# Kernel optimization log

Measured on AMD Instinct MI355X. Metric: run time of the kernel, lower is better.

Reference implementation:

```python
import jax, jax.numpy as jnp
from jax import lax
import numpy as np

C = 256       # residual_channels == skip_channels
B = 4
T = 4096
LATENT = 128
NB = 4        # n_blocks
NL = 10       # n_layers
ENC_DILS = tuple(2 ** i for i in range(NL)) * NB   # 40 encoder blocks
DEC_DILS = tuple(2 ** i for i in range(NL))        # 10 decoder blocks


def causal_conv(x, W, b, d):
    # x: [B, Cin, T], W: [Cout, Cin, k], left-pad by (k-1)*d for causality
    pad = (W.shape[-1] - 1) * d
    y = lax.conv_general_dilated(x, W, (1,), [(pad, 0)], rhs_dilation=(d,),
                                 dimension_numbers=('NCH', 'OIH', 'NCH'))
    return y + b[None, :, None]


def gated_block(h, Wf, bf, Wg, bg, Wr, br, Ws, bs, d):
    f = jnp.tanh(causal_conv(h, Wf, bf, d))
    g = jax.nn.sigmoid(causal_conv(h, Wg, bg, d))
    out = f * g
    res = jnp.einsum('oc,bct->bot', Wr, out) + br[None, :, None] + h
    skip = jnp.einsum('oc,bct->bot', Ws, out) + bs[None, :, None]
    return res, skip


def setup_inputs() -> dict:
    key = jax.random.key(0)
    ks = jax.random.split(key, 24)
    s = 0.05
    nE = NB * NL
    d = {}
    d['x'] = jax.random.normal(ks[0], (B, 1, T), jnp.float32)
    d['eps'] = jax.random.normal(ks[1], (B, LATENT), jnp.float32)
    d['enc_in_W'] = jax.random.normal(ks[2], (C, 1, 2)) * s
    d['enc_in_b'] = jnp.zeros((C,), jnp.float32)
    d['enc_Wf'] = jax.random.normal(ks[3], (nE, C, C, 2)) * s
    d['enc_bf'] = jnp.zeros((nE, C), jnp.float32)
    d['enc_Wg'] = jax.random.normal(ks[4], (nE, C, C, 2)) * s
    d['enc_bg'] = jnp.zeros((nE, C), jnp.float32)
    d['enc_Wr'] = jax.random.normal(ks[5], (nE, C, C)) * s
    d['enc_br'] = jnp.zeros((nE, C), jnp.float32)
    d['enc_Ws'] = jax.random.normal(ks[6], (nE, C, C)) * s
    d['enc_bs'] = jnp.zeros((nE, C), jnp.float32)
    d['fc_mu_W'] = jax.random.normal(ks[7], (LATENT, C)) * s
    d['fc_mu_b'] = jnp.zeros((LATENT,), jnp.float32)
    d['fc_lv_W'] = jax.random.normal(ks[8], (LATENT, C)) * s
    d['fc_lv_b'] = jnp.zeros((LATENT,), jnp.float32)
    d['dec_in_W'] = jax.random.normal(ks[9], (C, LATENT)) * s
    d['dec_in_b'] = jnp.zeros((C,), jnp.float32)
    d['dec_Wf'] = jax.random.normal(ks[10], (NL, C, C, 2)) * s
    d['dec_bf'] = jnp.zeros((NL, C), jnp.float32)
    d['dec_Wg'] = jax.random.normal(ks[11], (NL, C, C, 2)) * s
    d['dec_bg'] = jnp.zeros((NL, C), jnp.float32)
    d['dec_Wr'] = jax.random.normal(ks[12], (NL, C, C)) * s
    d['dec_br'] = jnp.zeros((NL, C), jnp.float32)
    d['out_W'] = jax.random.normal(ks[13], (1, C)) * s
    d['out_b'] = jnp.zeros((1,), jnp.float32)
    return d


def _forward(x, eps, enc_in_W, enc_in_b, enc_Wf, enc_bf, enc_Wg, enc_bg,
             enc_Wr, enc_br, enc_Ws, enc_bs, fc_mu_W, fc_mu_b, fc_lv_W, fc_lv_b,
             dec_in_W, dec_in_b, dec_Wf, dec_bf, dec_Wg, dec_bg, dec_Wr, dec_br,
             out_W, out_b):
    # --- encode ---
    h = causal_conv(x, enc_in_W, enc_in_b, 1)
    skip_sum = jnp.zeros((h.shape[0], C, h.shape[2]), h.dtype)
    for i, dil in enumerate(ENC_DILS):
        h, skip = gated_block(h, enc_Wf[i], enc_bf[i], enc_Wg[i], enc_bg[i],
                              enc_Wr[i], enc_br[i], enc_Ws[i], enc_bs[i], dil)
        skip_sum = skip_sum + skip
    pooled = skip_sum.mean(axis=-1)                      # [B, C]
    mu = pooled @ fc_mu_W.T + fc_mu_b                    # [B, LATENT]
    logvar = pooled @ fc_lv_W.T + fc_lv_b
    # --- reparameterize ---
    z = mu + eps * jnp.exp(0.5 * logvar)
    # --- decode (length-1 sequence) ---
    h2 = (jnp.einsum('ol,bl->bo', dec_in_W, z) + dec_in_b)[:, :, None]  # [B, C, 1]
    for i, dil in enumerate(DEC_DILS):
        f = jnp.tanh(causal_conv(h2, dec_Wf[i], dec_bf[i], dil))
        g = jax.nn.sigmoid(causal_conv(h2, dec_Wg[i], dec_bg[i], dil))
        out = f * g
        h2 = jnp.einsum('oc,bct->bot', dec_Wr[i], out) + dec_br[i][None, :, None] + h2
    y = jnp.einsum('oc,bct->bot', out_W, h2) + out_b[None, :, None]     # [B, 1, 1]
    return (y, mu, logvar)


def reference(x, eps, enc_in_W, enc_in_b, enc_Wf, enc_bf, enc_Wg, enc_bg,
              enc_Wr, enc_br, enc_Ws, enc_bs, fc_mu_W, fc_mu_b, fc_lv_W, fc_lv_b,
              dec_in_W, dec_in_b, dec_Wf, dec_bf, dec_Wg, dec_bg, dec_Wr, dec_br,
              out_W, out_b):
    return _forward(x, eps, enc_in_W, enc_in_b, enc_Wf, enc_bf, enc_Wg, enc_bg,
                    enc_Wr, enc_br, enc_Ws, enc_bs, fc_mu_W, fc_mu_b, fc_lv_W, fc_lv_b,
                    dec_in_W, dec_in_b, dec_Wf, dec_bf, dec_Wg, dec_bg, dec_Wr, dec_br,
                    out_W, out_b)
```

## Files before the change

### kernel.cpp

```cpp
#include <hip/hip_runtime.h>

typedef unsigned short u16;
typedef __attribute__((ext_vector_type(8))) __bf16 bf16x8;
typedef __attribute__((ext_vector_type(4))) float f32x4;

constexpr int C = 256;
constexpr int T = 4096;
constexpr int B = 4;
constexpr int NENC = 40;
constexpr int NDEC = 10;
constexpr int TILE = 64;

__device__ __forceinline__ float bf2f(u16 v) {
  union { unsigned u; float f; } x;
  x.u = ((unsigned)v) << 16;
  return x.f;
}
__device__ __forceinline__ u16 f2bf(float f) {
  union { float ff; unsigned u; } x;
  x.ff = f;
  unsigned r = x.u + 0x7fffu + ((x.u >> 16) & 1u);
  return (u16)(r >> 16);
}
__device__ __forceinline__ int swz(int row, int col) {
  int g = ((row & 7) ^ (row >> 3)) & 7;
  return row * 512 + (col ^ (g << 3));
}

typedef __attribute__((address_space(1))) const unsigned int* gp1_t;
typedef __attribute__((address_space(3))) unsigned int* lp3_t;
__device__ __forceinline__ void gl_lds16(const u16* g, u16* l) {
  __builtin_amdgcn_global_load_lds((gp1_t)(const void*)g, (lp3_t)(void*)l, 16, 0, 0);
}

__global__ void k_pack1(const float* __restrict__ Wf, const float* __restrict__ Wg,
                        u16* __restrict__ penc1, int total) {
  int p = blockIdx.x * 256 + threadIdx.x;
  if (p >= total) return;
  int lane = p & 63;
  int s = (p >> 6) & 3;
  int c = (p >> 8) & 15;
  int wv = (p >> 12) & 7;
  int layer = p >> 15;
  int co = wv * 32 + (s & 1) * 16 + (lane & 15);
  int k = c * 32 + (lane >> 4) * 8;
  const float* src = (s >= 2 ? Wg : Wf) + ((size_t)layer * C + co) * 512 + k;
  u16* dst = penc1 + (size_t)p * 8;
#pragma unroll
  for (int r = 0; r < 8; ++r) dst[r] = f2bf(src[r]);
}

__global__ void k_pack2(const float* __restrict__ Wr, u16* __restrict__ penc2, int total) {
  int p = blockIdx.x * 256 + threadIdx.x;
  if (p >= total) return;
  int lane = p & 63;
  int s = (p >> 6) & 1;
  int c = (p >> 7) & 7;
  int wv = (p >> 10) & 7;
  int layer = p >> 13;
  int co = wv * 32 + s * 16 + (lane & 15);
  int k = c * 32 + (lane >> 4) * 8;
  const float* src = Wr + ((size_t)layer * C + co) * 256 + k;
  u16* dst = penc2 + (size_t)p * 8;
#pragma unroll
  for (int r = 0; r < 8; ++r) dst[r] = f2bf(src[r]);
}

__global__ void k_packd(const float* __restrict__ dWf, const float* __restrict__ dWg,
                        const float* __restrict__ dWr, const float* __restrict__ dinW,
                        u16* __restrict__ pdfg, u16* __restrict__ pdr,
                        u16* __restrict__ tdin) {
  int p = blockIdx.x * 256 + threadIdx.x;
  if (p < 163840) {
    int lane = p & 63;
    int s = (p >> 6) & 1;
    int c = (p >> 7) & 7;
    int wv = (p >> 10) & 15;
    int layer = p >> 14;
    int co = wv * 16 + (lane & 15);
    int k = c * 32 + (lane >> 4) * 8;
    const float* src = (s ? dWg : dWf) + (((size_t)(layer * C + co)) * C + k) * 2 + 1;
    u16* dst = pdfg + (size_t)p * 8;
#pragma unroll
    for (int r = 0; r < 8; ++r) dst[r] = f2bf(src[2 * r]);
  } else if (p < 245760) {
    int q = p - 163840;
    int lane = q & 63;
    int c = (q >> 6) & 7;
    int wv = (q >> 9) & 15;
    int layer = q >> 13;
    int co = wv * 16 + (lane & 15);
    int k = c * 32 + (lane >> 4) * 8;
    const float* src = dWr + ((size_t)(layer * C + co)) * C + k;
    u16* dst = pdr + (size_t)q * 8;
#pragma unroll
    for (int r = 0; r < 8; ++r) dst[r] = f2bf(src[r]);
  } else if (p < 249856) {
    int u = p - 245760;
#pragma unroll
    for (int r = 0; r < 8; ++r) tdin[u * 8 + r] = f2bf(dinW[u * 8 + r]);
  }
}

__global__ void k_zero(float* __restrict__ p, int n) {
  int i = blockIdx.x * 256 + threadIdx.x;
  if (i < n) p[i] = 0.f;
}

__global__ void k_input(const float* __restrict__ x, const float* __restrict__ W,
                        const float* __restrict__ bin, float* __restrict__ h) {
  int idx = blockIdx.x * 256 + threadIdx.x;
  int t = idx & (T - 1);
  int c = (idx >> 12) & (C - 1);
  int b = idx >> 20;
  float xv = x[b * T + t];
  float xp = (t > 0) ? x[b * T + t - 1] : 0.f;
  h[idx] = W[2 * c] * xp + W[2 * c + 1] * xv + bin[c];
}

__global__ __launch_bounds__(512, 2) void k_enc(
    const float* __restrict__ hin, float* __restrict__ hout, float* __restrict__ rowsum_l,
    const u16* __restrict__ pw1, const float* __restrict__ bfb,
    const float* __restrict__ bgb,
    const u16* __restrict__ pw2, const float* __restrict__ brb,
    int dil) {
  extern __shared__ __align__(16) u16 smem[];
  u16* wb = smem + 64 * 512;
  const int tid = threadIdx.x;
  const int wave = tid >> 6;
  const int lane = tid & 63;
  const int ncol = lane & 15;
  const int quad = lane >> 4;
  const int wg = blockIdx.x;
  const int b = wg >> 6;
  const int t0 = (wg & 63) * TILE;
  const float* hb = hin + b * C * T;

  const int co0 = wave * 32;
  const int kq = quad * 8;
  const int off1 = (wg >> 3) & 15;
  const int off2 = (wg >> 3) & 7;
  const u16* b1 = pw1 + wave * 32768 + lane * 8;
  const u16* b2 = pw2 + wave * 8192 + lane * 8;
  u16* wreg0 = wb + wave * 2048;
  u16* wreg1 = wb + 16384 + wave * 2048;
  const int aoff = lane * 8;

#pragma unroll
  for (int cc = 0; cc < 2; ++cc) {
    u16* ld = cc ? wreg1 : wreg0;
    const u16* gs = b1 + ((off1 + cc) & 15) * 2048;
    gl_lds16(gs, ld);
    gl_lds16(gs + 512, ld + 512);
    gl_lds16(gs + 1024, ld + 1024);
    gl_lds16(gs + 1536, ld + 1536);
  }

  const int n4 = tid & 15;
  const int cib = tid >> 4;
  float4 v[16];
  const bool al4 = ((dil & 3) == 0);
  if (t0 >= dil) {
#pragma unroll
    for (int it2 = 0; it2 < 16; ++it2) {
      int ci = (cib + it2 * 32) & 255;
      int tap = it2 >> 3;
      int tb = t0 + n4 * 4 - (tap ? 0 : dil);
      const float* p = hb + ci * T + tb;
      if (tap || al4) {
        v[it2] = *(const float4*)p;
      } else {
        v[it2].x = p[0]; v[it2].y = p[1]; v[it2].z = p[2]; v[it2].w = p[3];
      }
    }
  } else {
#pragma unroll
    for (int it2 = 0; it2 < 16; ++it2) {
      int ci = (cib + it2 * 32) & 255;
      int tap = it2 >> 3;
      int tb = t0 + n4 * 4 - (tap ? 0 : dil);
      const float* p = hb + ci * T + tb;
      if (tap) {
        v[it2] = *(const float4*)p;
      } else {
        v[it2].x = (tb + 0 >= 0) ? p[0] : 0.f;
        v[it2].y = (tb + 1 >= 0) ? p[1] : 0.f;
        v[it2].z = (tb + 2 >= 0) ? p[2] : 0.f;
        v[it2].w = (tb + 3 >= 0) ? p[3] : 0.f;
      }
    }
  }
#pragma unroll
  for (int it2 = 0; it2 < 8; ++it2) {
    int ci = (cib + it2 * 32) & 255;
    const float* p0 = (const float*)&v[it2];
    const float* p1 = (const float*)&v[it2 + 8];
#pragma unroll
    for (int r = 0; r < 4; ++r) {
      unsigned w32 = (unsigned)f2bf(p0[r]) | ((unsigned)f2bf(p1[r]) << 16);
      *(unsigned*)(&smem[swz(n4 * 4 + r, 2 * ci)]) = w32;
    }
  }
  __syncthreads();

  f32x4 acc[4][4];
#pragma unroll
  for (int m = 0; m < 4; ++m)
#pragma unroll
    for (int nt = 0; nt < 4; ++nt)
      acc[m][nt] = (f32x4){0.f, 0.f, 0.f, 0.f};

#pragma unroll
  for (int c = 0; c < 16; ++c) {
    if (c < 15) asm volatile("s_waitcnt vmcnt(4)" ::: "memory");
    else        asm volatile("s_waitcnt vmcnt(0)" ::: "memory");
    const u16* wr_ = (c & 1) ? wreg1 : wreg0;
    bf16x8 af0 = *(const bf16x8*)(wr_ + aoff);
    bf16x8 af1 = *(const bf16x8*)(wr_ + 512 + aoff);
    bf16x8 af2 = *(const bf16x8*)(wr_ + 1024 + aoff);
    bf16x8 af3 = *(const bf16x8*)(wr_ + 1536 + aoff);
    const int kk = ((c + off1) & 15) * 32 + kq;
    bf16x8 bfr[4];
#pragma unroll
    for (int nt = 0; nt < 4; ++nt)
      bfr[nt] = *(const bf16x8*)(&smem[swz(nt * 16 + ncol, kk)]);
#pragma unroll
    for (int nt = 0; nt < 4; ++nt) {
      acc[0][nt] = __builtin_amdgcn_mfma_f32_16x16x32_bf16(af0, bfr[nt], acc[0][nt], 0, 0, 0);
      acc[1][nt] = __builtin_amdgcn_mfma_f32_16x16x32_bf16(af1, bfr[nt], acc[1][nt], 0, 0, 0);
      acc[2][nt] = __builtin_amdgcn_mfma_f32_16x16x32_bf16(af2, bfr[nt], acc[2][nt], 0, 0, 0);
      acc[3][nt] = __builtin_amdgcn_mfma_f32_16x16x32_bf16(af3, bfr[nt], acc[3][nt], 0, 0, 0);
    }
    if (c + 2 < 16) {
      asm volatile("s_waitcnt lgkmcnt(0)" ::: "memory");
      u16* ld = (c & 1) ? wreg1 : wreg0;
      const u16* gs = b1 + ((c + 2 + off1) & 15) * 2048;
      gl_lds16(gs, ld);
      gl_lds16(gs + 512, ld + 512);
      gl_lds16(gs + 1024, ld + 1024);
      gl_lds16(gs + 1536, ld + 1536);
    }
  }

#pragma unroll
  for (int cc = 0; cc < 2; ++cc) {
    u16* ld = cc ? wreg1 : wreg0;
    const u16* gs = b2 + ((off2 + cc) & 7) * 1024;
    gl_lds16(gs, ld);
    gl_lds16(gs + 512, ld + 512);
  }
  __syncthreads();

  float* rsb = rowsum_l + b * C;
#pragma unroll
  for (int j = 0; j < 2; ++j) {
    const int cob = co0 + j * 16 + quad * 4;
    float bfv[4], bgv[4], rs[4];
#pragma unroll
    for (int r = 0; r < 4; ++r) {
      bfv[r] = bfb[cob + r];
      bgv[r] = bgb[cob + r];
      rs[r] = 0.f;
    }
#pragma unroll
    for (int nt = 0; nt < 4; ++nt) {
      const int n = nt * 16 + ncol;
      u16 pk[4];
#pragma unroll
      for (int r = 0; r < 4; ++r) {
        float fv = acc[j][nt][r] + bfv[r];
        float gv = acc[2 + j][nt][r] + bgv[r];
        float th = 1.f - 2.f / (__expf(2.f * fv) + 1.f);
        float sg = 1.f / (1.f + __expf(-gv));
        float o = th * sg;
        rs[r] += o;
        pk[r] = f2bf(o);
      }
      uint2 w;
      w.x = (unsigned)pk[0] | ((unsigned)pk[1] << 16);
      w.y = (unsigned)pk[2] | ((unsigned)pk[3] << 16);
      *(uint2*)(&smem[swz(n, cob)]) = w;
    }
#pragma unroll
    for (int r = 0; r < 4; ++r) {
      float s = rs[r];
      s += __shfl_xor(s, 1);
      s += __shfl_xor(s, 2);
      s += __shfl_xor(s, 4);
      s += __shfl_xor(s, 8);
      if (ncol == 0) atomicAdd(&rsb[cob + r], s);
    }
  }
  __syncthreads();

  f32x4 acc2[2][4];
#pragma unroll
  for (int m = 0; m < 2; ++m)
#pragma unroll
    for (int nt = 0; nt < 4; ++nt)
      acc2[m][nt] = (f32x4){0.f, 0.f, 0.f, 0.f};

#pragma unroll
  for (int c = 0; c < 8; ++c) {
    if (c < 7) asm volatile("s_waitcnt vmcnt(2)" ::: "memory");
    else       asm volatile("s_waitcnt vmcnt(0)" ::: "memory");
    const u16* wr_ = (c & 1) ? wreg1 : wreg0;
    bf16x8 af0 = *(const bf16x8*)(wr_ + aoff);
    bf16x8 af1 = *(const bf16x8*)(wr_ + 512 + aoff);
    const int kk = ((c + off2) & 7) * 32 + kq;
    bf16x8 bfr[4];
#pragma unroll
    for (int nt = 0; nt < 4; ++nt)
      bfr[nt] = *(const bf16x8*)(&smem[swz(nt * 16 + ncol, kk)]);
#pragma unroll
    for (int nt = 0; nt < 4; ++nt) {
      acc2[0][nt] = __builtin_amdgcn_mfma_f32_16x16x32_bf16(af0, bfr[nt], acc2[0][nt], 0, 0, 0);
      acc2[1][nt] = __builtin_amdgcn_mfma_f32_16x16x32_bf16(af1, bfr[nt], acc2[1][nt], 0, 0, 0);
    }
    if (c + 2 < 8) {
      asm volatile("s_waitcnt lgkmcnt(0)" ::: "memory");
      u16* ld = (c & 1) ? wreg1 : wreg0;
      const u16* gs = b2 + ((c + 2 + off2) & 7) * 1024;
      gl_lds16(gs, ld);
      gl_lds16(gs + 512, ld + 512);
    }
  }
  __syncthreads();

  float* fb = (float*)smem;
#pragma unroll
  for (int m = 0; m < 2; ++m) {
    const int cob = co0 + m * 16 + quad * 4;
#pragma unroll
    for (int nt = 0; nt < 4; ++nt) {
      const int t = nt * 16 + ncol;
#pragma unroll
      for (int r = 0; r < 4; ++r)
        fb[(cob + r) * 66 + t] = acc2[m][nt][r] + brb[cob + r];
    }
  }
  __syncthreads();
  float* ho = hout + b * C * T;
#pragma unroll
  for (int it2 = 0; it2 < 8; ++it2) {
    const int ci = cib + it2 * 32;
    const float* fr = fb + ci * 66 + n4 * 4;
    float4 o;
    o.x = fr[0] + v[it2 + 8].x;
    o.y = fr[1] + v[it2 + 8].y;
    o.z = fr[2] + v[it2 + 8].z;
    o.w = fr[3] + v[it2 + 8].w;
    *(float4*)(ho + ci * T + t0 + n4 * 4) = o;
  }
}

__global__ __launch_bounds__(256) void k_skip(
    const float* __restrict__ encWs, const float* __restrict__ encbs,
    const float* __restrict__ rowsum, float* __restrict__ pooled) {
  __shared__ float rs[B][C];
  const int l = blockIdx.x;
  const int co = threadIdx.x;
  for (int i = co; i < B * C; i += 256) rs[i >> 8][i & 255] = rowsum[l * B * C + i];
  __syncthreads();
  const float* Wrow = encWs + (size_t)l * C * C + co * C;
  float bs = encbs[l * C + co] * (float)T;
  float d[B] = {0.f, 0.f, 0.f, 0.f};
  for (int ci = 0; ci < C; ci += 4) {
    float4 w = *(const float4*)(Wrow + ci);
#pragma unroll
    for (int b = 0; b < B; ++b)
      d[b] += w.x * rs[b][ci] + w.y * rs[b][ci + 1] + w.z * rs[b][ci + 2] + w.w * rs[b][ci + 3];
  }
#pragma unroll
  for (int b = 0; b < B; ++b) atomicAdd(&pooled[b * C + co], d[b] + bs);
}

__global__ __launch_bounds__(256) void k_fc(
    const float* __restrict__ pooled,
    const float* __restrict__ muW, const float* __restrict__ mub,
    const float* __restrict__ lvW, const float* __restrict__ lvb,
    float* __restrict__ mlbuf, float* __restrict__ dout) {
  __shared__ float pm[B * C];
  const int tid = threadIdx.x;
  for (int i = tid; i < B * C; i += 256) pm[i] = pooled[i] * (1.f / (float)T);
  __syncthreads();
  const int waveG = blockIdx.x * 4 + (tid >> 6);
  const int lane = tid & 63;
  for (int j = 0; j < 16; ++j) {
    int d = waveG * 16 + j;
    int b = d >> 8, r = d & 255, which = r >> 7, l = r & 127;
    const float* Wrow = (which ? lvW : muW) + l * C;
    const float* p = pm + b * C;
    float s = Wrow[lane] * p[lane] + Wrow[lane + 64] * p[lane + 64] +
              Wrow[lane + 128] * p[lane + 128] + Wrow[lane + 192] * p[lane + 192];
#pragma unroll
    for (int off = 32; off; off >>= 1) s += __shfl_xor(s, off);
    if (lane == 0) {
      float val = s + (which ? lvb[l] : mub[l]);
      mlbuf[which * 512 + b * 128 + l] = val;
      dout[4 + which * 512 + b * 128 + l] = val;
    }
  }
}

__global__ __launch_bounds__(1024, 1) void k_dec(
    const float* __restrict__ mlbuf, const float* __restrict__ eps,
    const u16* __restrict__ tdin, const float* __restrict__ dinb,
    const u16* __restrict__ pdfg, const float* __restrict__ dbf,
    const float* __restrict__ dbg,
    const u16* __restrict__ pdr, const float* __restrict__ dbr,
    const float* __restrict__ outW, const float* __restrict__ outb,
    float* __restrict__ dout) {
  extern __shared__ __align__(16) u16 dsm[];
  __shared__ __align__(16) u16 Ah[16][264];
  __shared__ __align__(16) u16 Ao[16][264];
  __shared__ float h2f[4][256];
  __shared__ float outred[4];
  const int tid = threadIdx.x;
  const int wave = tid >> 6;
  const int lane = tid & 63;
  const int ncol = lane & 15;
  const int quad = lane >> 4;
  const int kq = quad * 8;
  const int co = wave * 16 + ncol;
  u16* wreg = dsm + wave * 4096;

  bf16x8 tdw[4];
  {
    const u16* wp = tdin + co * 128;
#pragma unroll
    for (int it = 0; it < 4; ++it) tdw[it] = *(const bf16x8*)(wp + it * 32 + kq);
  }

  if (tid < 512) {
    int b = tid >> 7, l = tid & 127;
    float mu = mlbuf[b * 128 + l];
    float lv = mlbuf[512 + b * 128 + l];
    Ah[b][l] = f2bf(mu + eps[b * 128 + l] * expf(0.5f * lv));
  }
  if (tid < 4) outred[tid] = 0.f;
  __syncthreads();

  {
    f32x4 acch = (f32x4){0.f, 0.f, 0.f, 0.f};
#pragma unroll
    for (int it = 0; it < 4; ++it) {
      bf16x8 af = *(const bf16x8*)(&Ah[ncol][it * 32 + kq]);
      acch = __builtin_amdgcn_mfma_f32_16x16x32_bf16(af, tdw[it], acch, 0, 0, 0);
    }
    __syncthreads();
    if (quad == 0) {
      float bias = dinb[co];
#pragma unroll
      for (int r = 0; r < 4; ++r) {
        float hv = acch[r] + bias;
        h2f[r][co] = hv;
        Ah[r][co] = f2bf(hv);
      }
    }
  }
  {
    const u16* fb = pdfg + wave * 8192 + lane * 8;
#pragma unroll
    for (int cc = 0; cc < 4; ++cc) {
      gl_lds16(fb + cc * 1024, wreg + cc * 1024);
      gl_lds16(fb + cc * 1024 + 512, wreg + cc * 1024 + 512);
    }
  }
  __syncthreads();

  for (int i = 0; i < NDEC; ++i) {
    const u16* fb = pdfg + (i * 16 + wave) * 8192 + lane * 8;
    const u16* rb = pdr + (i * 16 + wave) * 4096 + lane * 8;

    f32x4 accf = (f32x4){0.f, 0.f, 0.f, 0.f};
    f32x4 accg = (f32x4){0.f, 0.f, 0.f, 0.f};
#pragma unroll
    for (int c = 0; c < 8; ++c) {
      if (c == 4) asm volatile("s_waitcnt vmcnt(6)" ::: "memory");
      else if (c == 5) asm volatile("s_waitcnt vmcnt(4)" ::: "memory");
      else if (c == 6) asm volatile("s_waitcnt vmcnt(2)" ::: "memory");
      else if (c == 7) asm volatile("s_waitcnt vmcnt(0)" ::: "memory");
      const u16* bufp = wreg + (c & 3) * 1024;
      bf16x8 bf_ = *(const bf16x8*)(bufp + lane * 8);
      bf16x8 bg_ = *(const bf16x8*)(bufp + 512 + lane * 8);
      bf16x8 af = *(const bf16x8*)(&Ah[ncol][c * 32 + kq]);
      accf = __builtin_amdgcn_mfma_f32_16x16x32_bf16(af, bf_, accf, 0, 0, 0);
      accg = __builtin_amdgcn_mfma_f32_16x16x32_bf16(af, bg_, accg, 0, 0, 0);
      if (c < 4) {
        asm volatile("s_waitcnt lgkmcnt(0)" ::: "memory");
        gl_lds16(fb + (c + 4) * 1024, wreg + (c & 3) * 1024);
        gl_lds16(fb + (c + 4) * 1024 + 512, wreg + (c & 3) * 1024 + 512);
      }
    }
    asm volatile("s_waitcnt lgkmcnt(0)" ::: "memory");
#pragma unroll
    for (int cc = 0; cc < 4; ++cc) gl_lds16(rb + cc * 512, wreg + cc * 1024);

    if (quad == 0) {
      float bfv = dbf[i * C + co];
      float bgv = dbg[i * C + co];
#pragma unroll
      for (int r = 0; r < 4; ++r) {
        float fv = accf[r] + bfv;
        float gv = accg[r] + bgv;
        float th = 1.f - 2.f / (__expf(2.f * fv) + 1.f);
        float sg = 1.f / (1.f + __expf(-gv));
        Ao[r][co] = f2bf(th * sg);
      }
    }
    __syncthreads();

    f32x4 accr = (f32x4){0.f, 0.f, 0.f, 0.f};
#pragma unroll
    for (int c = 0; c < 8; ++c) {
      if (c == 4) asm volatile("s_waitcnt vmcnt(3)" ::: "memory");
      else if (c == 5) asm volatile("s_waitcnt vmcnt(2)" ::: "memory");
      else if (c == 6) asm volatile("s_waitcnt vmcnt(1)" ::: "memory");
      else if (c == 7) asm volatile("s_waitcnt vmcnt(0)" ::: "memory");
      bf16x8 br_ = *(const bf16x8*)(wreg + (c & 3) * 1024 + lane * 8);
      bf16x8 af = *(const bf16x8*)(&Ao[ncol][c * 32 + kq]);
      accr = __builtin_amdgcn_mfma_f32_16x16x32_bf16(af, br_, accr, 0, 0, 0);
      if (c < 4) {
        asm volatile("s_waitcnt lgkmcnt(0)" ::: "memory");
        gl_lds16(rb + (c + 4) * 512, wreg + (c & 3) * 1024);
      }
    }
    if (i + 1 < NDEC) {
      const u16* nfb = pdfg + ((i + 1) * 16 + wave) * 8192 + lane * 8;
      asm volatile("s_waitcnt lgkmcnt(0)" ::: "memory");
#pragma unroll
      for (int cc = 0; cc < 4; ++cc) {
        gl_lds16(nfb + cc * 1024, wreg + cc * 1024);
        gl_lds16(nfb + cc * 1024 + 512, wreg + cc * 1024 + 512);
      }
    }
    if (quad == 0) {
      float brv = dbr[i * C + co];
#pragma unroll
      for (int r = 0; r < 4; ++r) {
        float hv = h2f[r][co] + accr[r] + brv;
        h2f[r][co] = hv;
        Ah[r][co] = f2bf(hv);
      }
    }
    __syncthreads();
  }

  {
    int b = tid >> 8, c = tid & 255;
    float val = outW[c] * h2f[b][c];
#pragma unroll
    for (int off = 32; off; off >>= 1) val += __shfl_xor(val, off);
    if (lane == 0) atomicAdd(&outred[b], val);
  }
  __syncthreads();
  if (tid < 4) dout[tid] = outred[tid] + outb[0];
}

extern "C" void kernel_launch(void* const* d_in, const int* in_sizes, int n_in,
                              void* d_out, int out_size, void* d_ws, size_t ws_size,
                              hipStream_t stream) {
  const float* x      = (const float*)d_in[0];
  const float* eps    = (const float*)d_in[1];
  const float* encinW = (const float*)d_in[2];
  const float* encinb = (const float*)d_in[3];
  const float* encWf  = (const float*)d_in[4];
  const float* encbf  = (const float*)d_in[5];
  const float* encWg  = (const float*)d_in[6];
  const float* encbg  = (const float*)d_in[7];
  const float* encWr  = (const float*)d_in[8];
  const float* encbr  = (const float*)d_in[9];
  const float* encWs  = (const float*)d_in[10];
  const float* encbs  = (const float*)d_in[11];
  const float* muW    = (const float*)d_in[12];
  const float* mub    = (const float*)d_in[13];
  const float* lvW    = (const float*)d_in[14];
  const float* lvb    = (const float*)d_in[15];
  const float* dinW   = (const float*)d_in[16];
  const float* dinb   = (const float*)d_in[17];
  const float* dWf    = (const float*)d_in[18];
  const float* dbf    = (const float*)d_in[19];
  const float* dWg    = (const float*)d_in[20];
  const float* dbg    = (const float*)d_in[21];
  const float* dWr    = (const float*)d_in[22];
  const float* dbr    = (const float*)d_in[23];
  const float* outW   = (const float*)d_in[24];
  const float* outb   = (const float*)d_in[25];
  float* dout = (float*)d_out;

  char* ws = (char*)d_ws;
  float* hA = (float*)ws;
  float* hB = hA + (size_t)B * C * T;
  float* pooled = hB + (size_t)B * C * T;
  float* mlbuf = pooled + B * C;
  float* rowsum = mlbuf + 1024;
  u16* penc1 = (u16*)(rowsum + NENC * B * C);
  u16* penc2 = penc1 + (size_t)10485760;
  u16* pdfg = penc2 + (size_t)2621440;
  u16* pdr = pdfg + (size_t)1310720;
  u16* tdin = pdr + (size_t)655360;

  (void)hipFuncSetAttribute(reinterpret_cast<const void*>(k_enc),
                            hipFuncAttributeMaxDynamicSharedMemorySize, 131072);
  (void)hipFuncSetAttribute(reinterpret_cast<const void*>(k_dec),
                            hipFuncAttributeMaxDynamicSharedMemorySize, 131072);

  k_pack1<<<(1310720 + 255) / 256, 256, 0, stream>>>(encWf, encWg, penc1, 1310720);
  k_pack2<<<(327680 + 255) / 256, 256, 0, stream>>>(encWr, penc2, 327680);
  k_packd<<<(249856 + 255) / 256, 256, 0, stream>>>(dWf, dWg, dWr, dinW, pdfg, pdr, tdin);

  const int nZ = B * C + 1024 + NENC * B * C;
  k_zero<<<(nZ + 255) / 256, 256, 0, stream>>>(pooled, nZ);
  k_input<<<(B * C * T) / 256, 256, 0, stream>>>(x, encinW, encinb, hA);

  for (int i = 0; i < NENC; ++i) {
    const int dil = 1 << (i % 10);
    const float* hi = (i & 1) ? hB : hA;
    float* ho = (i & 1) ? hA : hB;
    k_enc<<<256, 512, 131072, stream>>>(
        hi, ho, rowsum + (size_t)i * B * C,
        penc1 + (size_t)i * 262144, encbf + (size_t)i * C,
        encbg + (size_t)i * C,
        penc2 + (size_t)i * 65536, encbr + (size_t)i * C,
        dil);
  }

  k_skip<<<NENC, 256, 0, stream>>>(encWs, encbs, rowsum, pooled);
  k_fc<<<16, 256, 0, stream>>>(pooled, muW, mub, lvW, lvb, mlbuf, dout);
  k_dec<<<1, 1024, 131072, stream>>>(mlbuf, eps, tdin, dinb, pdfg, dbf, dbg,
                                     pdr, dbr, outW, outb, dout);
}
```

Measured before the change: 1.287 ms.

## Spread decoder across 16 blocks with global barriers and packed bf16 converts

Replaces the single-block MFMA decoder with a 16-block kernel where each block owns 16 output channels, computes scalar dot products from register-held bf16 weights, and exchanges gate outputs and hidden state through global memory with an atomic grid barrier per half-layer. Decoder weights are repacked into a new transposed layout to match this access pattern. The encoder's bf16 conversions are replaced with the hardware packed convert instruction. This aims to cut the serial decoder latency by using more CUs, at the cost of 20 global barriers and a reliance on all 16 blocks being co-resident.

```diff
diff --git a/kernel.cpp b/kernel.cpp
--- a/kernel.cpp
+++ b/kernel.cpp
@@ -72,29 +72,36 @@
                         u16* __restrict__ tdin) {
   int p = blockIdx.x * 256 + threadIdx.x;
   if (p < 163840) {
-    int lane = p & 63;
-    int s = (p >> 6) & 1;
-    int c = (p >> 7) & 7;
-    int wv = (p >> 10) & 15;
-    int layer = p >> 14;
-    int co = wv * 16 + (lane & 15);
-    int k = c * 32 + (lane >> 4) * 8;
-    const float* src = (s ? dWg : dWf) + (((size_t)(layer * C + co)) * C + k) * 2 + 1;
-    u16* dst = pdfg + (size_t)p * 8;
-#pragma unroll
-    for (int r = 0; r < 8; ++r) dst[r] = f2bf(src[2 * r]);
+    int e0 = p * 8;
+    int layer = e0 >> 17;
+    int rem = e0 & 131071;
+    int co = rem >> 9;
+    int q = rem & 511;
+    int which = q >> 8;
+    int pos0 = q & 255;
+    const float* src = (which ? dWg : dWf) + ((size_t)(layer * 256 + co)) * 512 + 1;
+    u16* dst = pdfg + e0;
+#pragma unroll
+    for (int r = 0; r < 8; ++r) {
+      int pos = pos0 + r;
+      int k = ((pos & 15) << 4) | (pos >> 4);
+      dst[r] = f2bf(src[2 * k]);
+    }
   } else if (p < 245760) {
     int q = p - 163840;
-    int lane = q & 63;
-    int c = (q >> 6) & 7;
-    int wv = (q >> 9) & 15;
-    int layer = q >> 13;
-    int co = wv * 16 + (lane & 15);
-    int k = c * 32 + (lane >> 4) * 8;
-    const float* src = dWr + ((size_t)(layer * C + co)) * C + k;
-    u16* dst = pdr + (size_t)q * 8;
-#pragma unroll
-    for (int r = 0; r < 8; ++r) dst[r] = f2bf(src[r]);
+    int e0 = q * 8;
+    int layer = e0 >> 16;
+    int rem = e0 & 65535;
+    int co = rem >> 8;
+    int pos0 = rem & 255;
+    const float* src = dWr + ((size_t)(layer * 256 + co)) * 256;
+    u16* dst = pdr + e0;
+#pragma unroll
+    for (int r = 0; r < 8; ++r) {
+      int pos = pos0 + r;
+      int k = ((pos & 15) << 4) | (pos >> 4);
+      dst[r] = f2bf(src[k]);
+    }
   } else if (p < 249856) {
     int u = p - 245760;
 #pragma unroll
@@ -197,7 +204,8 @@
     const float* p1 = (const float*)&v[it2 + 8];
 #pragma unroll
     for (int r = 0; r < 4; ++r) {
-      unsigned w32 = (unsigned)f2bf(p0[r]) | ((unsigned)f2bf(p1[r]) << 16);
+      unsigned w32;
+      asm("v_cvt_pk_bf16_f32 %0, %1, %2" : "=v"(w32) : "v"(p0[r]), "v"(p1[r]));
       *(unsigned*)(&smem[swz(n4 * 4 + r, 2 * ci)]) = w32;
     }
   }
@@ -255,7 +263,7 @@
 #pragma unroll
   for (int j = 0; j < 2; ++j) {
     const int cob = co0 + j * 16 + quad * 4;
-    float bfv[4], bgv[4], rs[4];
+    float bfv[4], bgv[4], rs[4], ov[4];
 #pragma unroll
     for (int r = 0; r < 4; ++r) {
       bfv[r] = bfb[cob + r];
@@ -265,7 +273,6 @@
 #pragma unroll
     for (int nt = 0; nt < 4; ++nt) {
       const int n = nt * 16 + ncol;
-      u16 pk[4];
 #pragma unroll
       for (int r = 0; r < 4; ++r) {
         float fv = acc[j][nt][r] + bfv[r];
@@ -274,11 +281,11 @@
         float sg = 1.f / (1.f + __expf(-gv));
         float o = th * sg;
         rs[r] += o;
-        pk[r] = f2bf(o);
+        ov[r] = o;
       }
       uint2 w;
-      w.x = (unsigned)pk[0] | ((unsigned)pk[1] << 16);
-      w.y = (unsigned)pk[2] | ((unsigned)pk[3] << 16);
+      asm("v_cvt_pk_bf16_f32 %0, %1, %2" : "=v"(w.x) : "v"(ov[0]), "v"(ov[1]));
+      asm("v_cvt_pk_bf16_f32 %0, %1, %2" : "=v"(w.y) : "v"(ov[2]), "v"(ov[3]));
       *(uint2*)(&smem[swz(n, cob)]) = w;
     }
 #pragma unroll
@@ -403,159 +410,169 @@
   }
 }
 
-__global__ __launch_bounds__(1024, 1) void k_dec(
+struct WSet { uint4 f0, f1, g0, g1; };
+__device__ __forceinline__ WSet load_fg(const u16* __restrict__ pdfg, int L, int co, int kofs) {
+  const u16* pf = pdfg + ((size_t)(L * 256 + co)) * 512 + kofs * 16;
+  WSet s;
+  s.f0 = *(const uint4*)pf;
+  s.f1 = *(const uint4*)(pf + 8);
+  s.g0 = *(const uint4*)(pf + 256);
+  s.g1 = *(const uint4*)(pf + 264);
+  return s;
+}
+__device__ __forceinline__ float gate_fn(float fv, float gv) {
+  float th = 1.f - 2.f / (__expf(2.f * fv) + 1.f);
+  float sg = 1.f / (1.f + __expf(-gv));
+  return th * sg;
+}
+__device__ __forceinline__ void gbar_sync(int* __restrict__ bar, int idx, int nblk) {
+  __threadfence();
+  __syncthreads();
+  if (threadIdx.x == 0) {
+    __hip_atomic_fetch_add(&bar[idx], 1, __ATOMIC_ACQ_REL, __HIP_MEMORY_SCOPE_AGENT);
+    while (__hip_atomic_load(&bar[idx], __ATOMIC_ACQUIRE, __HIP_MEMORY_SCOPE_AGENT) < nblk)
+      __builtin_amdgcn_s_sleep(1);
+  }
+  __syncthreads();
+}
+
+#define DOT16(a0, a1, a2, a3, W0, W1, S)                                   \
+  do {                                                                     \
+    const unsigned uu[8] = {W0.x, W0.y, W0.z, W0.w, W1.x, W1.y, W1.z, W1.w}; \
+    _Pragma("unroll") for (int m = 0; m < 8; ++m) {                        \
+      float wl = bf2f((u16)(uu[m] & 0xffffu));                             \
+      float wh = bf2f((u16)(uu[m] >> 16));                                 \
+      int k0 = kofs + 32 * m, k1 = k0 + 16;                                \
+      a0 += wl * S[0][k0] + wh * S[0][k1];                                 \
+      a1 += wl * S[1][k0] + wh * S[1][k1];                                 \
+      a2 += wl * S[2][k0] + wh * S[2][k1];                                 \
+      a3 += wl * S[3][k0] + wh * S[3][k1];                                 \
+    }                                                                      \
+  } while (0)
+
+#define RED16(x)            \
+  do {                      \
+    x += __shfl_xor(x, 1);  \
+    x += __shfl_xor(x, 2);  \
+    x += __shfl_xor(x, 4);  \
+    x += __shfl_xor(x, 8);  \
+  } while (0)
+
+__global__ __launch_bounds__(256, 1) void k_dec2(
     const float* __restrict__ mlbuf, const float* __restrict__ eps,
     const u16* __restrict__ tdin, const float* __restrict__ dinb,
     const u16* __restrict__ pdfg, const float* __restrict__ dbf,
     const float* __restrict__ dbg,
     const u16* __restrict__ pdr, const float* __restrict__ dbr,
     const float* __restrict__ outW, const float* __restrict__ outb,
-    float* __restrict__ dout) {
-  extern __shared__ __align__(16) u16 dsm[];
-  __shared__ __align__(16) u16 Ah[16][264];
-  __shared__ __align__(16) u16 Ao[16][264];
-  __shared__ float h2f[4][256];
-  __shared__ float outred[4];
+    float* __restrict__ dout, int* __restrict__ gbar,
+    float* __restrict__ gout, float* __restrict__ gh) {
+  __shared__ float zs[4][128];
+  __shared__ float hs[4][256];
+  __shared__ float os[4][256];
+  __shared__ float red[4][4];
   const int tid = threadIdx.x;
-  const int wave = tid >> 6;
-  const int lane = tid & 63;
-  const int ncol = lane & 15;
-  const int quad = lane >> 4;
-  const int kq = quad * 8;
-  const int co = wave * 16 + ncol;
-  u16* wreg = dsm + wave * 4096;
-
-  bf16x8 tdw[4];
+  const int blk = blockIdx.x;
+  const int kofs = tid & 15;
+  const int co = blk * 16 + (tid >> 4);
+
+  for (int u = tid; u < 512; u += 256) {
+    int b = u >> 7, l = u & 127;
+    zs[b][l] = mlbuf[b * 128 + l] + eps[b * 128 + l] * expf(0.5f * mlbuf[512 + b * 128 + l]);
+  }
+  __syncthreads();
+
   {
-    const u16* wp = tdin + co * 128;
-#pragma unroll
-    for (int it = 0; it < 4; ++it) tdw[it] = *(const bf16x8*)(wp + it * 32 + kq);
-  }
-
-  if (tid < 512) {
-    int b = tid >> 7, l = tid & 127;
-    float mu = mlbuf[b * 128 + l];
-    float lv = mlbuf[512 + b * 128 + l];
-    Ah[b][l] = f2bf(mu + eps[b * 128 + l] * expf(0.5f * lv));
-  }
-  if (tid < 4) outred[tid] = 0.f;
-  __syncthreads();
-
-  {
-    f32x4 acch = (f32x4){0.f, 0.f, 0.f, 0.f};
-#pragma unroll
-    for (int it = 0; it < 4; ++it) {
-      bf16x8 af = *(const bf16x8*)(&Ah[ncol][it * 32 + kq]);
-      acch = __builtin_amdgcn_mfma_f32_16x16x32_bf16(af, tdw[it], acch, 0, 0, 0);
-    }
+    float a0 = 0.f, a1 = 0.f, a2 = 0.f, a3 = 0.f;
+    const u16* wp = tdin + tid * 128;
+#pragma unroll 4
+    for (int k = 0; k < 128; k += 2) {
+      unsigned ww = *(const unsigned*)(wp + k);
+      float w0 = bf2f((u16)(ww & 0xffffu)), w1 = bf2f((u16)(ww >> 16));
+      a0 += w0 * zs[0][k] + w1 * zs[0][k + 1];
+      a1 += w0 * zs[1][k] + w1 * zs[1][k + 1];
+      a2 += w0 * zs[2][k] + w1 * zs[2][k + 1];
+      a3 += w0 * zs[3][k] + w1 * zs[3][k + 1];
+    }
+    float bi = dinb[tid];
+    hs[0][tid] = a0 + bi;
+    hs[1][tid] = a1 + bi;
+    hs[2][tid] = a2 + bi;
+    hs[3][tid] = a3 + bi;
+  }
+  __syncthreads();
+
+  WSet cur = load_fg(pdfg, 0, co, kofs);
+  for (int i = 0; i < NDEC; ++i) {
+    const u16* pr = pdr + ((size_t)(i * 256 + co)) * 256 + kofs * 16;
+    uint4 rw0 = *(const uint4*)pr;
+    uint4 rw1 = *(const uint4*)(pr + 8);
+
+    float f0 = 0.f, f1 = 0.f, f2 = 0.f, f3 = 0.f;
+    float g0 = 0.f, g1 = 0.f, g2 = 0.f, g3 = 0.f;
+    DOT16(f0, f1, f2, f3, cur.f0, cur.f1, hs);
+    DOT16(g0, g1, g2, g3, cur.g0, cur.g1, hs);
+    WSet nxt = load_fg(pdfg, (i + 1 < NDEC) ? i + 1 : NDEC - 1, co, kofs);
+    RED16(f0); RED16(f1); RED16(f2); RED16(f3);
+    RED16(g0); RED16(g1); RED16(g2); RED16(g3);
+    float bfv = dbf[i * 256 + co], bgv = dbg[i * 256 + co];
+    float o0 = gate_fn(f0 + bfv, g0 + bgv);
+    float o1 = gate_fn(f1 + bfv, g1 + bgv);
+    float o2 = gate_fn(f2 + bfv, g2 + bgv);
+    float o3 = gate_fn(f3 + bfv, g3 + bgv);
+    {
+      int r = tid & 15;
+      float ov = r == 0 ? o0 : r == 1 ? o1 : r == 2 ? o2 : o3;
+      if (r < 4) gout[r * 256 + co] = ov;
+    }
+    gbar_sync(gbar, 2 * i, 16);
+#pragma unroll
+    for (int u = 0; u < 4; ++u)
+      os[u][tid] = __hip_atomic_load(&gout[tid + u * 256], __ATOMIC_RELAXED,
+                                     __HIP_MEMORY_SCOPE_AGENT);
     __syncthreads();
-    if (quad == 0) {
-      float bias = dinb[co];
-#pragma unroll
-      for (int r = 0; r < 4; ++r) {
-        float hv = acch[r] + bias;
-        h2f[r][co] = hv;
-        Ah[r][co] = f2bf(hv);
-      }
-    }
-  }
-  {
-    const u16* fb = pdfg + wave * 8192 + lane * 8;
-#pragma unroll
-    for (int cc = 0; cc < 4; ++cc) {
-      gl_lds16(fb + cc * 1024, wreg + cc * 1024);
-      gl_lds16(fb + cc * 1024 + 512, wreg + cc * 1024 + 512);
-    }
-  }
-  __syncthreads();
-
-  for (int i = 0; i < NDEC; ++i) {
-    const u16* fb = pdfg + (i * 16 + wave) * 8192 + lane * 8;
-    const u16* rb = pdr + (i * 16 + wave) * 4096 + lane * 8;
-
-    f32x4 accf = (f32x4){0.f, 0.f, 0.f, 0.f};
-    f32x4 accg = (f32x4){0.f, 0.f, 0.f, 0.f};
-#pragma unroll
-    for (int c = 0; c < 8; ++c) {
-      if (c == 4) asm volatile("s_waitcnt vmcnt(6)" ::: "memory");
-      else if (c == 5) asm volatile("s_waitcnt vmcnt(4)" ::: "memory");
-      else if (c == 6) asm volatile("s_waitcnt vmcnt(2)" ::: "memory");
-      else if (c == 7) asm volatile("s_waitcnt vmcnt(0)" ::: "memory");
-      const u16* bufp = wreg + (c & 3) * 1024;
-      bf16x8 bf_ = *(const bf16x8*)(bufp + lane * 8);
-      bf16x8 bg_ = *(const bf16x8*)(bufp + 512 + lane * 8);
-      bf16x8 af = *(const bf16x8*)(&Ah[ncol][c * 32 + kq]);
-      accf = __builtin_amdgcn_mfma_f32_16x16x32_bf16(af, bf_, accf, 0, 0, 0);
-      accg = __builtin_amdgcn_mfma_f32_16x16x32_bf16(af, bg_, accg, 0, 0, 0);
-      if (c < 4) {
-        asm volatile("s_waitcnt lgkmcnt(0)" ::: "memory");
-        gl_lds16(fb + (c + 4) * 1024, wreg + (c & 3) * 1024);
-        gl_lds16(fb + (c + 4) * 1024 + 512, wreg + (c & 3) * 1024 + 512);
-      }
-    }
-    asm volatile("s_waitcnt lgkmcnt(0)" ::: "memory");
-#pragma unroll
-    for (int cc = 0; cc < 4; ++cc) gl_lds16(rb + cc * 512, wreg + cc * 1024);
-
-    if (quad == 0) {
-      float bfv = dbf[i * C + co];
-      float bgv = dbg[i * C + co];
-#pragma unroll
-      for (int r = 0; r < 4; ++r) {
-        float fv = accf[r] + bfv;
-        float gv = accg[r] + bgv;
-        float th = 1.f - 2.f / (__expf(2.f * fv) + 1.f);
-        float sg = 1.f / (1.f + __expf(-gv));
-        Ao[r][co] = f2bf(th * sg);
-      }
-    }
+
+    float r0 = 0.f, r1 = 0.f, r2 = 0.f, r3 = 0.f;
+    DOT16(r0, r1, r2, r3, rw0, rw1, os);
+    RED16(r0); RED16(r1); RED16(r2); RED16(r3);
+    float brv = dbr[i * 256 + co];
+    float h0 = hs[0][co] + r0 + brv;
+    float h1 = hs[1][co] + r1 + brv;
+    float h2 = hs[2][co] + r2 + brv;
+    float h3 = hs[3][co] + r3 + brv;
+    {
+      int r = tid & 15;
+      float hv = r == 0 ? h0 : r == 1 ? h1 : r == 2 ? h2 : h3;
+      if (r < 4) gh[r * 256 + co] = hv;
+    }
+    gbar_sync(gbar, 2 * i + 1, 16);
+#pragma unroll
+    for (int u = 0; u < 4; ++u)
+      hs[u][tid] = __hip_atomic_load(&gh[tid + u * 256], __ATOMIC_RELAXED,
+                                     __HIP_MEMORY_SCOPE_AGENT);
     __syncthreads();
-
-    f32x4 accr = (f32x4){0.f, 0.f, 0.f, 0.f};
-#pragma unroll
-    for (int c = 0; c < 8; ++c) {
-      if (c == 4) asm volatile("s_waitcnt vmcnt(3)" ::: "memory");
-      else if (c == 5) asm volatile("s_waitcnt vmcnt(2)" ::: "memory");
-      else if (c == 6) asm volatile("s_waitcnt vmcnt(1)" ::: "memory");
-      else if (c == 7) asm volatile("s_waitcnt vmcnt(0)" ::: "memory");
-      bf16x8 br_ = *(const bf16x8*)(wreg + (c & 3) * 1024 + lane * 8);
-      bf16x8 af = *(const bf16x8*)(&Ao[ncol][c * 32 + kq]);
-      accr = __builtin_amdgcn_mfma_f32_16x16x32_bf16(af, br_, accr, 0, 0, 0);
-      if (c < 4) {
-        asm volatile("s_waitcnt lgkmcnt(0)" ::: "memory");
-        gl_lds16(rb + (c + 4) * 512, wreg + (c & 3) * 1024);
-      }
-    }
-    if (i + 1 < NDEC) {
-      const u16* nfb = pdfg + ((i + 1) * 16 + wave) * 8192 + lane * 8;
-      asm volatile("s_waitcnt lgkmcnt(0)" ::: "memory");
-#pragma unroll
-      for (int cc = 0; cc < 4; ++cc) {
-        gl_lds16(nfb + cc * 1024, wreg + cc * 1024);
-        gl_lds16(nfb + cc * 1024 + 512, wreg + cc * 1024 + 512);
-      }
-    }
-    if (quad == 0) {
-      float brv = dbr[i * C + co];
-#pragma unroll
-      for (int r = 0; r < 4; ++r) {
-        float hv = h2f[r][co] + accr[r] + brv;
-        h2f[r][co] = hv;
-        Ah[r][co] = f2bf(hv);
-      }
+    cur = nxt;
+  }
+
+  if (blk == 0) {
+    float w = outW[tid];
+    float v0 = w * hs[0][tid], v1 = w * hs[1][tid];
+    float v2 = w * hs[2][tid], v3 = w * hs[3][tid];
+#pragma unroll
+    for (int off = 32; off; off >>= 1) {
+      v0 += __shfl_xor(v0, off);
+      v1 += __shfl_xor(v1, off);
+      v2 += __shfl_xor(v2, off);
+      v3 += __shfl_xor(v3, off);
+    }
+    if ((tid & 63) == 0) {
+      int wv = tid >> 6;
+      red[wv][0] = v0; red[wv][1] = v1; red[wv][2] = v2; red[wv][3] = v3;
     }
     __syncthreads();
-  }
-
-  {
-    int b = tid >> 8, c = tid & 255;
-    float val = outW[c] * h2f[b][c];
-#pragma unroll
-    for (int off = 32; off; off >>= 1) val += __shfl_xor(val, off);
-    if (lane == 0) atomicAdd(&outred[b], val);
-  }
-  __syncthreads();
-  if (tid < 4) dout[tid] = outred[tid] + outb[0];
+    if (tid < 4)
+      dout[tid] = red[0][tid] + red[1][tid] + red[2][tid] + red[3][tid] + outb[0];
+  }
 }
 
 extern "C" void kernel_launch(void* const* d_in, const int* in_sizes, int n_in,
@@ -594,7 +611,10 @@
   float* hB = hA + (size_t)B * C * T;
   float* pooled = hB + (size_t)B * C * T;
   float* mlbuf = pooled + B * C;
-  float* rowsum = mlbuf + 1024;
+  int* gbar = (int*)(mlbuf + 1024);
+  float* goutb = (float*)(gbar + 32);
+  float* ghb = goutb + 1024;
+  float* rowsum = ghb + 1024;
   u16* penc1 = (u16*)(rowsum + NENC * B * C);
   u16* penc2 = penc1 + (size_t)10485760;
   u16* pdfg = penc2 + (size_t)2621440;
@@ -603,14 +623,12 @@
 
   (void)hipFuncSetAttribute(reinterpret_cast<const void*>(k_enc),
                             hipFuncAttributeMaxDynamicSharedMemorySize, 131072);
-  (void)hipFuncSetAttribute(reinterpret_cast<const void*>(k_dec),
-                            hipFuncAttributeMaxDynamicSharedMemorySize, 131072);
 
   k_pack1<<<(1310720 + 255) / 256, 256, 0, stream>>>(encWf, encWg, penc1, 1310720);
   k_pack2<<<(327680 + 255) / 256, 256, 0, stream>>>(encWr, penc2, 327680);
   k_packd<<<(249856 + 255) / 256, 256, 0, stream>>>(dWf, dWg, dWr, dinW, pdfg, pdr, tdin);
 
-  const int nZ = B * C + 1024 + NENC * B * C;
+  const int nZ = 1024 + 1024 + 2080 + NENC * B * C;
   k_zero<<<(nZ + 255) / 256, 256, 0, stream>>>(pooled, nZ);
   k_input<<<(B * C * T) / 256, 256, 0, stream>>>(x, encinW, encinb, hA);
 
@@ -628,6 +646,6 @@
 
   k_skip<<<NENC, 256, 0, stream>>>(encWs, encbs, rowsum, pooled);
   k_fc<<<16, 256, 0, stream>>>(pooled, muW, mub, lvW, lvb, mlbuf, dout);
-  k_dec<<<1, 1024, 131072, stream>>>(mlbuf, eps, tdin, dinb, pdfg, dbf, dbg,
-                                     pdr, dbr, outW, outb, dout);
-}
+  k_dec2<<<16, 256, 0, stream>>>(mlbuf, eps, tdin, dinb, pdfg, dbf, dbg,
+                                 pdr, dbr, outW, outb, dout, gbar, goutb, ghb);
+}
```

Result: slower. 1.355 ms (+5.3%).

## Split encoder block across 16 waves with direct register weight prefetch

Applied to the files above, without the earlier changes.

The encoder kernel now launches 1024 threads per block instead of 512, so each wave owns 16 output channels rather than 32 and keeps half as many accumulators. Weight fragments are loaded straight from global memory into registers, double-buffered one chunk ahead, instead of being staged through LDS with async copies. This cuts dynamic LDS from 128 KB to about 66 KB. The aim is more waves per CU to hide latency and no LDS weight staging. The cost is a shallower prefetch and more exposed global latency. The tight launch-bounds hint may also force register spills.

```diff
diff --git a/kernel.cpp b/kernel.cpp
--- a/kernel.cpp
+++ b/kernel.cpp
@@ -118,14 +118,13 @@
   h[idx] = W[2 * c] * xp + W[2 * c + 1] * xv + bin[c];
 }
 
-__global__ __launch_bounds__(512, 2) void k_enc(
+__global__ __launch_bounds__(1024, 4) void k_enc(
     const float* __restrict__ hin, float* __restrict__ hout, float* __restrict__ rowsum_l,
     const u16* __restrict__ pw1, const float* __restrict__ bfb,
     const float* __restrict__ bgb,
     const u16* __restrict__ pw2, const float* __restrict__ brb,
     int dil) {
   extern __shared__ __align__(16) u16 smem[];
-  u16* wb = smem + 64 * 512;
   const int tid = threadIdx.x;
   const int wave = tid >> 6;
   const int lane = tid & 63;
@@ -136,89 +135,77 @@
   const int t0 = (wg & 63) * TILE;
   const float* hb = hin + b * C * T;
 
-  const int co0 = wave * 32;
+  const int co0 = wave * 16;
   const int kq = quad * 8;
   const int off1 = (wg >> 3) & 15;
   const int off2 = (wg >> 3) & 7;
-  const u16* b1 = pw1 + wave * 32768 + lane * 8;
-  const u16* b2 = pw2 + wave * 8192 + lane * 8;
-  u16* wreg0 = wb + wave * 2048;
-  u16* wreg1 = wb + 16384 + wave * 2048;
-  const int aoff = lane * 8;
-
-#pragma unroll
-  for (int cc = 0; cc < 2; ++cc) {
-    u16* ld = cc ? wreg1 : wreg0;
-    const u16* gs = b1 + ((off1 + cc) & 15) * 2048;
-    gl_lds16(gs, ld);
-    gl_lds16(gs + 512, ld + 512);
-    gl_lds16(gs + 1024, ld + 1024);
-    gl_lds16(gs + 1536, ld + 1536);
-  }
+  const u16* b1w = pw1 + (wave >> 1) * 32768 + (wave & 1) * 512 + lane * 8;
+  const u16* b2w = pw2 + (wave >> 1) * 8192 + (wave & 1) * 512 + lane * 8;
 
   const int n4 = tid & 15;
   const int cib = tid >> 4;
-  float4 v[16];
+  float4 v0[4], v1[4];
   const bool al4 = ((dil & 3) == 0);
   if (t0 >= dil) {
 #pragma unroll
-    for (int it2 = 0; it2 < 16; ++it2) {
-      int ci = (cib + it2 * 32) & 255;
-      int tap = it2 >> 3;
-      int tb = t0 + n4 * 4 - (tap ? 0 : dil);
+    for (int j = 0; j < 4; ++j) {
+      int ci = cib + j * 64;
+      const float* p = hb + ci * T + t0 + n4 * 4 - dil;
+      if (al4) {
+        v0[j] = *(const float4*)p;
+      } else {
+        v0[j].x = p[0]; v0[j].y = p[1]; v0[j].z = p[2]; v0[j].w = p[3];
+      }
+      v1[j] = *(const float4*)(hb + ci * T + t0 + n4 * 4);
+    }
+  } else {
+#pragma unroll
+    for (int j = 0; j < 4; ++j) {
+      int ci = cib + j * 64;
+      int tb = t0 + n4 * 4 - dil;
       const float* p = hb + ci * T + tb;
-      if (tap || al4) {
-        v[it2] = *(const float4*)p;
-      } else {
-        v[it2].x = p[0]; v[it2].y = p[1]; v[it2].z = p[2]; v[it2].w = p[3];
-      }
-    }
-  } else {
-#pragma unroll
-    for (int it2 = 0; it2 < 16; ++it2) {
-      int ci = (cib + it2 * 32) & 255;
-      int tap = it2 >> 3;
-      int tb = t0 + n4 * 4 - (tap ? 0 : dil);
-      const float* p = hb + ci * T + tb;
-      if (tap) {
-        v[it2] = *(const float4*)p;
-      } else {
-        v[it2].x = (tb + 0 >= 0) ? p[0] : 0.f;
-        v[it2].y = (tb + 1 >= 0) ? p[1] : 0.f;
-        v[it2].z = (tb + 2 >= 0) ? p[2] : 0.f;
-        v[it2].w = (tb + 3 >= 0) ? p[3] : 0.f;
-      }
-    }
-  }
-#pragma unroll
-  for (int it2 = 0; it2 < 8; ++it2) {
-    int ci = (cib + it2 * 32) & 255;
-    const float* p0 = (const float*)&v[it2];
-    const float* p1 = (const float*)&v[it2 + 8];
+      v0[j].x = (tb + 0 >= 0) ? p[0] : 0.f;
+      v0[j].y = (tb + 1 >= 0) ? p[1] : 0.f;
+      v0[j].z = (tb + 2 >= 0) ? p[2] : 0.f;
+      v0[j].w = (tb + 3 >= 0) ? p[3] : 0.f;
+      v1[j] = *(const float4*)(hb + ci * T + t0 + n4 * 4);
+    }
+  }
+#pragma unroll
+  for (int j = 0; j < 4; ++j) {
+    int ci = cib + j * 64;
+    const float* p0 = (const float*)&v0[j];
+    const float* p1 = (const float*)&v1[j];
 #pragma unroll
     for (int r = 0; r < 4; ++r) {
       unsigned w32 = (unsigned)f2bf(p0[r]) | ((unsigned)f2bf(p1[r]) << 16);
       *(unsigned*)(&smem[swz(n4 * 4 + r, 2 * ci)]) = w32;
     }
   }
-  __syncthreads();
-
-  f32x4 acc[4][4];
-#pragma unroll
-  for (int m = 0; m < 4; ++m)
+
+  bf16x8 wf[2], wg_[2];
+  {
+    const u16* gs = b1w + (off1 & 15) * 2048;
+    wf[0] = *(const bf16x8*)gs;
+    wg_[0] = *(const bf16x8*)(gs + 1024);
+  }
+  __syncthreads();
+
+  f32x4 acc[2][4];
+#pragma unroll
+  for (int m = 0; m < 2; ++m)
 #pragma unroll
     for (int nt = 0; nt < 4; ++nt)
       acc[m][nt] = (f32x4){0.f, 0.f, 0.f, 0.f};
 
-#pragma unroll
+#pragma unroll 2
   for (int c = 0; c < 16; ++c) {
-    if (c < 15) asm volatile("s_waitcnt vmcnt(4)" ::: "memory");
-    else        asm volatile("s_waitcnt vmcnt(0)" ::: "memory");
-    const u16* wr_ = (c & 1) ? wreg1 : wreg0;
-    bf16x8 af0 = *(const bf16x8*)(wr_ + aoff);
-    bf16x8 af1 = *(const bf16x8*)(wr_ + 512 + aoff);
-    bf16x8 af2 = *(const bf16x8*)(wr_ + 1024 + aoff);
-    bf16x8 af3 = *(const bf16x8*)(wr_ + 1536 + aoff);
+    const int cb = c & 1;
+    if (c < 15) {
+      const u16* gs = b1w + ((c + 1 + off1) & 15) * 2048;
+      wf[cb ^ 1] = *(const bf16x8*)gs;
+      wg_[cb ^ 1] = *(const bf16x8*)(gs + 1024);
+    }
     const int kk = ((c + off1) & 15) * 32 + kq;
     bf16x8 bfr[4];
 #pragma unroll
@@ -226,35 +213,21 @@
       bfr[nt] = *(const bf16x8*)(&smem[swz(nt * 16 + ncol, kk)]);
 #pragma unroll
     for (int nt = 0; nt < 4; ++nt) {
-      acc[0][nt] = __builtin_amdgcn_mfma_f32_16x16x32_bf16(af0, bfr[nt], acc[0][nt], 0, 0, 0);
-      acc[1][nt] = __builtin_amdgcn_mfma_f32_16x16x32_bf16(af1, bfr[nt], acc[1][nt], 0, 0, 0);
-      acc[2][nt] = __builtin_amdgcn_mfma_f32_16x16x32_bf16(af2, bfr[nt], acc[2][nt], 0, 0, 0);
-      acc[3][nt] = __builtin_amdgcn_mfma_f32_16x16x32_bf16(af3, bfr[nt], acc[3][nt], 0, 0, 0);
-    }
-    if (c + 2 < 16) {
-      asm volatile("s_waitcnt lgkmcnt(0)" ::: "memory");
-      u16* ld = (c & 1) ? wreg1 : wreg0;
-      const u16* gs = b1 + ((c + 2 + off1) & 15) * 2048;
-      gl_lds16(gs, ld);
-      gl_lds16(gs + 512, ld + 512);
-      gl_lds16(gs + 1024, ld + 1024);
-      gl_lds16(gs + 1536, ld + 1536);
-    }
-  }
-
-#pragma unroll
-  for (int cc = 0; cc < 2; ++cc) {
-    u16* ld = cc ? wreg1 : wreg0;
-    const u16* gs = b2 + ((off2 + cc) & 7) * 1024;
-    gl_lds16(gs, ld);
-    gl_lds16(gs + 512, ld + 512);
+      acc[0][nt] = __builtin_amdgcn_mfma_f32_16x16x32_bf16(wf[cb], bfr[nt], acc[0][nt], 0, 0, 0);
+      acc[1][nt] = __builtin_amdgcn_mfma_f32_16x16x32_bf16(wg_[cb], bfr[nt], acc[1][nt], 0, 0, 0);
+    }
+  }
+
+  bf16x8 w2[2];
+  {
+    const u16* gs = b2w + (off2 & 7) * 1024;
+    w2[0] = *(const bf16x8*)gs;
   }
   __syncthreads();
 
   float* rsb = rowsum_l + b * C;
-#pragma unroll
-  for (int j = 0; j < 2; ++j) {
-    const int cob = co0 + j * 16 + quad * 4;
+  {
+    const int cob = co0 + quad * 4;
     float bfv[4], bgv[4], rs[4];
 #pragma unroll
     for (int r = 0; r < 4; ++r) {
@@ -268,8 +241,8 @@
       u16 pk[4];
 #pragma unroll
       for (int r = 0; r < 4; ++r) {
-        float fv = acc[j][nt][r] + bfv[r];
-        float gv = acc[2 + j][nt][r] + bgv[r];
+        float fv = acc[0][nt][r] + bfv[r];
+        float gv = acc[1][nt][r] + bgv[r];
         float th = 1.f - 2.f / (__expf(2.f * fv) + 1.f);
         float sg = 1.f / (1.f + __expf(-gv));
         float o = th * sg;
@@ -293,63 +266,51 @@
   }
   __syncthreads();
 
-  f32x4 acc2[2][4];
-#pragma unroll
-  for (int m = 0; m < 2; ++m)
-#pragma unroll
-    for (int nt = 0; nt < 4; ++nt)
-      acc2[m][nt] = (f32x4){0.f, 0.f, 0.f, 0.f};
-
-#pragma unroll
+  f32x4 acc2[4];
+#pragma unroll
+  for (int nt = 0; nt < 4; ++nt)
+    acc2[nt] = (f32x4){0.f, 0.f, 0.f, 0.f};
+
+#pragma unroll 2
   for (int c = 0; c < 8; ++c) {
-    if (c < 7) asm volatile("s_waitcnt vmcnt(2)" ::: "memory");
-    else       asm volatile("s_waitcnt vmcnt(0)" ::: "memory");
-    const u16* wr_ = (c & 1) ? wreg1 : wreg0;
-    bf16x8 af0 = *(const bf16x8*)(wr_ + aoff);
-    bf16x8 af1 = *(const bf16x8*)(wr_ + 512 + aoff);
+    const int cb = c & 1;
+    if (c < 7) {
+      const u16* gs = b2w + ((c + 1 + off2) & 7) * 1024;
+      w2[cb ^ 1] = *(const bf16x8*)gs;
+    }
     const int kk = ((c + off2) & 7) * 32 + kq;
     bf16x8 bfr[4];
 #pragma unroll
     for (int nt = 0; nt < 4; ++nt)
       bfr[nt] = *(const bf16x8*)(&smem[swz(nt * 16 + ncol, kk)]);
 #pragma unroll
-    for (int nt = 0; nt < 4; ++nt) {
-      acc2[0][nt] = __builtin_amdgcn_mfma_f32_16x16x32_bf16(af0, bfr[nt], acc2[0][nt], 0, 0, 0);
-      acc2[1][nt] = __builtin_amdgcn_mfma_f32_16x16x32_bf16(af1, bfr[nt], acc2[1][nt], 0, 0, 0);
-    }
-    if (c + 2 < 8) {
-      asm volatile("s_waitcnt lgkmcnt(0)" ::: "memory");
-      u16* ld = (c & 1) ? wreg1 : wreg0;
-      const u16* gs = b2 + ((c + 2 + off2) & 7) * 1024;
-      gl_lds16(gs, ld);
-      gl_lds16(gs + 512, ld + 512);
-    }
+    for (int nt = 0; nt < 4; ++nt)
+      acc2[nt] = __builtin_amdgcn_mfma_f32_16x16x32_bf16(w2[cb], bfr[nt], acc2[nt], 0, 0, 0);
   }
   __syncthreads();
 
   float* fb = (float*)smem;
-#pragma unroll
-  for (int m = 0; m < 2; ++m) {
-    const int cob = co0 + m * 16 + quad * 4;
+  {
+    const int cob = co0 + quad * 4;
 #pragma unroll
     for (int nt = 0; nt < 4; ++nt) {
       const int t = nt * 16 + ncol;
 #pragma unroll
       for (int r = 0; r < 4; ++r)
-        fb[(cob + r) * 66 + t] = acc2[m][nt][r] + brb[cob + r];
+        fb[(cob + r) * 66 + t] = acc2[nt][r] + brb[cob + r];
     }
   }
   __syncthreads();
   float* ho = hout + b * C * T;
 #pragma unroll
-  for (int it2 = 0; it2 < 8; ++it2) {
-    const int ci = cib + it2 * 32;
+  for (int j = 0; j < 4; ++j) {
+    const int ci = cib + j * 64;
     const float* fr = fb + ci * 66 + n4 * 4;
     float4 o;
-    o.x = fr[0] + v[it2 + 8].x;
-    o.y = fr[1] + v[it2 + 8].y;
-    o.z = fr[2] + v[it2 + 8].z;
-    o.w = fr[3] + v[it2 + 8].w;
+    o.x = fr[0] + v1[j].x;
+    o.y = fr[1] + v1[j].y;
+    o.z = fr[2] + v1[j].z;
+    o.w = fr[3] + v1[j].w;
     *(float4*)(ho + ci * T + t0 + n4 * 4) = o;
   }
 }
@@ -602,7 +563,7 @@
   u16* tdin = pdr + (size_t)655360;
 
   (void)hipFuncSetAttribute(reinterpret_cast<const void*>(k_enc),
-                            hipFuncAttributeMaxDynamicSharedMemorySize, 131072);
+                            hipFuncAttributeMaxDynamicSharedMemorySize, 67584);
   (void)hipFuncSetAttribute(reinterpret_cast<const void*>(k_dec),
                             hipFuncAttributeMaxDynamicSharedMemorySize, 131072);
 
@@ -618,7 +579,7 @@
     const int dil = 1 << (i % 10);
     const float* hi = (i & 1) ? hB : hA;
     float* ho = (i & 1) ? hA : hB;
-    k_enc<<<256, 512, 131072, stream>>>(
+    k_enc<<<256, 1024, 67584, stream>>>(
         hi, ho, rowsum + (size_t)i * B * C,
         penc1 + (size_t)i * 262144, encbf + (size_t)i * C,
         encbg + (size_t)i * C,
```

Result: slower. 1.395 ms (+8.4%).
